# Optimization experiments

Hardware: AMD Instinct MI355X
Metric: run time of the kernel (lower is better)

## Reference

```python
import math
import jax, jax.numpy as jnp
import numpy as np
from jax import lax

N_HEADS = 8
FACTOR = 5


def _pos_emb(L, d):
    pos = jnp.arange(L, dtype=jnp.float32)[:, None]
    div = jnp.exp(jnp.arange(0, d, 2, dtype=jnp.float32) * (-math.log(10000.0) / d))
    pe = jnp.zeros((L, d), jnp.float32)
    pe = pe.at[:, 0::2].set(jnp.sin(pos * div))
    pe = pe.at[:, 1::2].set(jnp.cos(pos * div))
    return pe


def _circ_conv1d(x, w, b=None):
    # x: (B, L, Cin); w: torch conv1d weight (Cout, Cin, 3); circular padding=1
    xp = jnp.concatenate([x[:, -1:], x, x[:, :1]], axis=1)
    y = lax.conv_general_dilated(xp, jnp.transpose(w, (2, 1, 0)), (1,), 'VALID',
                                 dimension_numbers=('NWC', 'WIO', 'NWC'))
    return y + b if b is not None else y


def _ln(x, g, b, eps=1e-5):
    mu = x.mean(-1, keepdims=True)
    var = ((x - mu) ** 2).mean(-1, keepdims=True)
    return (x - mu) * lax.rsqrt(var + eps) * g + b


def _prob_attn(q, k, v, key):
    # q,k,v: (b, h, L, d); self-attention so l_q == l_k == L
    b, h, L, d = q.shape
    u = min(L, int(FACTOR * math.log(L + 1)))  # sample_k == n_top
    idx = jnp.asarray(jax.random.randint(key, (L, u), 0, L))  # shared across b,h as in torch

    # sampled QK scores: scan over the u samples to avoid a (b,h,L,u,d) gather blow-up
    def step(_, idx_s):
        kg = k[:, :, idx_s]  # (b,h,L,d): key idx_s[l] for query l
        return None, jnp.einsum('bhld,bhld->bhl', q, kg)
    _, qk = lax.scan(step, None, idx.T)  # (u, b, h, L)
    qk = jnp.moveaxis(qk, 0, -1)  # (b, h, L, u)

    m = qk.max(axis=-1) - qk.mean(axis=-1)  # sparsity measure, (b,h,L)
    _, top = lax.top_k(m, u)  # (b,h,u) top-u query indices

    q_red = jnp.take_along_axis(q, top[..., None], axis=2)  # (b,h,u,d)
    scores = jnp.einsum('bhud,bhkd->bhuk', q_red, k) * (1.0 / math.sqrt(d))
    attn = jax.nn.softmax(scores, axis=-1)
    ctx_top = jnp.einsum('bhuk,bhkd->bhud', attn, v)

    # non-selected queries get mean(V); scatter sparse-attention rows back in
    ctx = jnp.broadcast_to(v.mean(axis=2, keepdims=True), (b, h, L, d))
    bi = jnp.arange(b)[:, None, None]
    hi = jnp.arange(h)[None, :, None]
    return ctx.at[bi, hi, top].set(ctx_top)


def _attn_layer(x, wq, bq, wk, bk, wv, bv, wo, bo, key):
    b, L, dm = x.shape
    dh = dm // N_HEADS
    def split(w_, b_):
        return (x @ w_.T + b_).reshape(b, L, N_HEADS, dh).transpose(0, 2, 1, 3)
    ctx = _prob_attn(split(wq, bq), split(wk, bk), split(wv, bv), key)
    ctx = ctx.transpose(0, 2, 1, 3).reshape(b, L, dm)
    return ctx @ wo.T + bo


def _conv_layer(x, w, b, g, beta):
    # circular conv -> BatchNorm (batch stats, train-mode math) -> ELU -> maxpool k3 s2 p1
    y = _circ_conv1d(x, w, b)
    mu = y.mean(axis=(0, 1))
    var = y.var(axis=(0, 1))
    y = (y - mu) * lax.rsqrt(var + 1e-5) * g + beta
    y = jax.nn.elu(y)
    yp = jnp.pad(y, ((0, 0), (1, 1), (0, 0)), constant_values=-np.inf)
    return lax.reduce_window(yp, -np.inf, lax.max, (1, 3, 1), (1, 2, 1), 'VALID')


def _forward(x, skip_w, skip_b, token_conv_w, wq, bq, wk, bk, wv, bv, wo, bo,
             w1, b1, w2, b2, ln1_g, ln1_b, ln2_g, ln2_b,
             dc_w, dc_b, bn_g, bn_b, final_ln_g, final_ln_b, proj_w, proj_b):
    skip = x[:, -1] @ skip_w.T + skip_b  # (B, pred_len)
    h = _circ_conv1d(x, token_conv_w)  # token embedding (no bias)
    h = h + _pos_emb(h.shape[1], h.shape[2])
    E = wq.shape[0]
    base = jax.random.key(42)
    for i in range(E):
        new_h = _attn_layer(h, wq[i], bq[i], wk[i], bk[i], wv[i], bv[i], wo[i], bo[i],
                            jax.random.fold_in(base, i))
        h = h + new_h
        y = _ln(h, ln1_g[i], ln1_b[i])
        y = jax.nn.gelu(y @ w1[i].T + b1[i], approximate=False)  # conv1 is 1x1
        y = y @ w2[i].T + b2[i]  # conv2 is 1x1
        h = _ln(h + y, ln2_g[i], ln2_b[i])
        if i < E - 1:
            h = _conv_layer(h, dc_w[i], dc_b[i], bn_g[i], bn_b[i])  # halves L
    h = _ln(h, final_ln_g, final_ln_b)
    return h[:, -1] @ proj_w.T + proj_b + skip


def setup_inputs() -> dict:
    B, L, C_IN, D, DFF, E, P = 32, 2048, 7, 512, 2048, 3, 96
    key = jax.random.key(0)
    ks = iter(jax.random.split(key, 20))
    w = lambda shape: jax.random.normal(next(ks), shape, jnp.float32) * 0.02
    z = lambda shape: jnp.zeros(shape, jnp.float32)
    o = lambda shape: jnp.ones(shape, jnp.float32)
    return {
        'x': jax.random.normal(next(ks), (B, L, C_IN), jnp.float32),
        'skip_w': w((P, C_IN)), 'skip_b': z((P,)),
        'token_conv_w': w((D, C_IN, 3)),
        'wq': w((E, D, D)), 'bq': z((E, D)),
        'wk': w((E, D, D)), 'bk': z((E, D)),
        'wv': w((E, D, D)), 'bv': z((E, D)),
        'wo': w((E, D, D)), 'bo': z((E, D)),
        'w1': w((E, DFF, D)), 'b1': z((E, DFF)),
        'w2': w((E, D, DFF)), 'b2': z((E, D)),
        'ln1_g': o((E, D)), 'ln1_b': z((E, D)),
        'ln2_g': o((E, D)), 'ln2_b': z((E, D)),
        'dc_w': w((E - 1, D, D, 3)), 'dc_b': z((E - 1, D)),
        'bn_g': o((E - 1, D)), 'bn_b': z((E - 1, D)),
        'final_ln_g': o((D,)), 'final_ln_b': z((D,)),
        'proj_w': w((P, D)), 'proj_b': z((P,)),
    }


def reference(x, skip_w, skip_b, token_conv_w, wq, bq, wk, bk, wv, bv, wo, bo,
              w1, b1, w2, b2, ln1_g, ln1_b, ln2_g, ln2_b,
              dc_w, dc_b, bn_g, bn_b, final_ln_g, final_ln_b, proj_w, proj_b):
    return _forward(x, skip_w, skip_b, token_conv_w, wq, bq, wk, bk, wv, bv, wo, bo,
                    w1, b1, w2, b2, ln1_g, ln1_b, ln2_g, ln2_b,
                    dc_w, dc_b, bn_g, bn_b, final_ln_g, final_ln_b, proj_w, proj_b)
```

## Files before the change

### kernel.cpp

```cpp
#include <hip/hip_runtime.h>
#include <cmath>

#define DM 512
#define DH 64

typedef __attribute__((ext_vector_type(8))) short short8;
typedef __attribute__((ext_vector_type(4))) float float4v;

__device__ inline float b2f(unsigned short u){
  union{unsigned int i; float f;} z; z.i = ((unsigned)u)<<16; return z.f;
}
__device__ inline unsigned short f2b(float f){
  unsigned int x = __float_as_uint(f);
  return (unsigned short)((x + 0x7fffu + ((x>>16)&1u)) >> 16);
}

#define GLL(gp, lp) __builtin_amdgcn_global_load_lds((const __attribute__((address_space(1))) void*)(gp), \
    (__attribute__((address_space(3))) void*)(lp), 16, 0, 0)

__host__ __device__ inline void tf2x32(unsigned k0, unsigned k1, unsigned& x0, unsigned& x1){
  const unsigned ks0=k0, ks1=k1, ks2=k0^k1^0x1BD11BDAu;
  x0 += ks0; x1 += ks1;
#define TF_ROT(r) { x0 += x1; x1 = (x1<<(r))|(x1>>(32-(r))); x1 ^= x0; }
  TF_ROT(13) TF_ROT(15) TF_ROT(26) TF_ROT(6)
  x0 += ks1; x1 += ks2 + 1u;
  TF_ROT(17) TF_ROT(29) TF_ROT(16) TF_ROT(24)
  x0 += ks2; x1 += ks0 + 2u;
  TF_ROT(13) TF_ROT(15) TF_ROT(26) TF_ROT(6)
  x0 += ks0; x1 += ks1 + 3u;
  TF_ROT(17) TF_ROT(29) TF_ROT(16) TF_ROT(24)
  x0 += ks1; x1 += ks2 + 4u;
  TF_ROT(13) TF_ROT(15) TF_ROT(26) TF_ROT(6)
  x0 += ks2; x1 += ks0 + 5u;
#undef TF_ROT
}

__global__ __launch_bounds__(256) void idx_kernel(int* __restrict__ idx, unsigned k2a, unsigned k2b,
                                                  int S2, int Lmask){
  int j = blockIdx.x*256 + threadIdx.x;
  if (j >= S2) return;
  unsigned x0 = (unsigned)j, x1 = (unsigned)(S2 + j);
  tf2x32(k2a, k2b, x0, x1);
  idx[j]      = (int)(x0 & (unsigned)Lmask);
  idx[S2 + j] = (int)(x1 & (unsigned)Lmask);
}

__global__ __launch_bounds__(256) void pe_kernel(float* __restrict__ pe, int L){
  int i = blockIdx.x*256 + threadIdx.x;
  int d = i % DM, l = i / DM;
  const float scale = -0.017988946f;
  float freq = expf((float)(d & ~1) * scale);
  float ang  = (float)l * freq;
  pe[i] = (d & 1) ? cosf(ang) : sinf(ang);
}

__global__ __launch_bounds__(256) void embed_kernel(const float* __restrict__ x, const float* __restrict__ tcw,
                                                    const float* __restrict__ pe, float* __restrict__ h, int L){
  size_t i = (size_t)blockIdx.x*256 + threadIdx.x;
  int d = (int)(i % DM);
  size_t r = i / DM;
  int l = (int)(r % L);
  int b = (int)(r / L);
  const float* xb = x + (size_t)b*L*7;
  float acc = 0.f;
#pragma unroll
  for (int kk=0; kk<3; kk++){
    int ls = l + kk - 1;
    ls = (ls < 0) ? ls + L : (ls >= L ? ls - L : ls);
    const float* xe = xb + (size_t)ls*7;
    const float* wp = tcw + (size_t)d*21 + kk;
#pragma unroll
    for (int c=0;c<7;c++) acc += xe[c]*wp[3*c];
  }
  h[i] = acc + pe[(size_t)l*DM + d];
}

__global__ __launch_bounds__(256) void f2b_vec(const float* __restrict__ src, unsigned short* __restrict__ dst, int n4){
  int i = blockIdx.x*256 + threadIdx.x;
  if (i >= n4) return;
  float4 v = ((const float4*)src)[i];
  ushort4 o; o.x = f2b(v.x); o.y = f2b(v.y); o.z = f2b(v.z); o.w = f2b(v.w);
  ((ushort4*)dst)[i] = o;
}

__global__ __launch_bounds__(256) void packconv(const float* __restrict__ dcw, unsigned short* __restrict__ wtapK){
  int i = blockIdx.x*256 + threadIdx.x;
  if (i >= 3*DM*DM) return;
  int n = i / (3*DM); int rem = i % (3*DM); int tap = rem / DM; int c = rem % DM;
  wtapK[(size_t)n*(3*DM) + tap*DM + c] = f2b(dcw[((size_t)n*DM + c)*3 + tap]);
}

__global__ __launch_bounds__(256) void catb_kernel(const float* __restrict__ a, const float* __restrict__ b,
    const float* __restrict__ c, float* __restrict__ o){
  int i = blockIdx.x*256 + threadIdx.x;
  if (i >= 1536) return;
  o[i] = (i < 512) ? a[i] : (i < 1024 ? b[i-512] : c[i-1024]);
}

template<int TN, int A32>
__global__ __launch_bounds__(256) void bgemm2(const void* __restrict__ Ain,
    const unsigned short* __restrict__ Wb, const float* __restrict__ bias, void* __restrict__ C,
    int N, int K, int L, int convmode, int act, int outbf, int qkv, size_t bufstride, int swz){
  constexpr int NJ = TN/32;
  constexpr int BR = TN/32;
  __shared__ unsigned short As[128*64];
  __shared__ unsigned short Bs[TN*64];
  int tid = threadIdx.x;
  int w = tid >> 6, ln = tid & 63;

  int bx = blockIdx.x, by = blockIdx.y;
  if (swz){
    int XT = gridDim.x, YT = gridDim.y;
    int lid = by*XT + bx;
    int xcd = lid & 7, s = lid >> 3;
    int ych = YT >> 3;
    int CHv = ych < 16 ? ych : 16;
    int yloc = s % CHv;
    int t2 = s / CHv;
    int xx = t2 % XT;
    int chunk = t2 / XT;
    by = xcd*ych + chunk*CHv + yloc;
    bx = xx;
  }
  int row0 = by*128, col0 = bx*TN;
  int KA = convmode ? 512 : K;

  long aBase[4], dPrev[4], dNext[4]; int aCol[4];
#pragma unroll
  for (int g=0; g<4; g++){
    int ch = g*256 + tid;
    int r = ch >> 3, c = ch & 7;
    int gc = c ^ (r & 7);
    int gr = row0 + r;
    aCol[g] = gc*8;
    aBase[g] = (long)gr * KA;
    if (convmode){
      int l = gr % L;
      dPrev[g] = (l==0)   ? (long)(L-1)*KA : -(long)KA;
      dNext[g] = (l==L-1) ? -(long)(L-1)*KA : (long)KA;
    } else { dPrev[g]=0; dNext[g]=0; }
  }
  long bBase[BR];
#pragma unroll
  for (int g=0; g<BR; g++){
    int ch = g*256 + tid;
    int r = ch >> 3, c = ch & 7;
    int gc = c ^ (r & 7);
    bBase[g] = (long)(col0 + r)*K + gc*8;
  }
  int raBase[4], rbBase[NJ];
#pragma unroll
  for (int i=0;i<4;i++)  raBase[i] = ((w&1)*64 + i*16 + (ln&15))*8;
#pragma unroll
  for (int j=0;j<NJ;j++) rbBase[j] = ((w>>1)*(TN/2) + j*16 + (ln&15))*8;

  float4v acc[4][NJ] = {};
  int nIter = K/64;
  const unsigned short* A16 = (const unsigned short*)Ain;
  const float* Af = (const float*)Ain;

  for (int it=0; it<nIter; it++){
    int k0 = it*64;
    int kk = convmode ? (k0 & 511) : k0;
    int seg = convmode ? (k0 >> 9) : 1;
    if (A32){
#pragma unroll
      for (int g=0; g<4; g++){
        long d = convmode ? ((seg==0) ? dPrev[g] : (seg==2 ? dNext[g] : 0)) : 0;
        const float* src = Af + aBase[g] + d + kk + aCol[g];
        float4 v0 = *(const float4*)src;
        float4 v1 = *(const float4*)(src+4);
        short8 pk;
        pk[0]=(short)f2b(v0.x); pk[1]=(short)f2b(v0.y); pk[2]=(short)f2b(v0.z); pk[3]=(short)f2b(v0.w);
        pk[4]=(short)f2b(v1.x); pk[5]=(short)f2b(v1.y); pk[6]=(short)f2b(v1.z); pk[7]=(short)f2b(v1.w);
        *(short8*)((char*)As + g*4096 + tid*16) = pk;
      }
    } else {
#pragma unroll
      for (int g=0; g<4; g++){
        long d = convmode ? ((seg==0) ? dPrev[g] : (seg==2 ? dNext[g] : 0)) : 0;
        GLL(A16 + aBase[g] + d + kk + aCol[g], (char*)As + g*4096 + w*1024);
      }
    }
#pragma unroll
    for (int g=0; g<BR; g++)
      GLL(Wb + bBase[g] + k0, (char*)Bs + g*4096 + w*1024);
    __syncthreads();
    const char* ab = (const char*)As;
    const char* bb = (const char*)Bs;
#pragma unroll
    for (int s=0;s<2;s++){
      int xs = (s*4 + (ln>>4)) ^ (ln&7);
      short8 af[4], bf[NJ];
#pragma unroll
      for (int i=0;i<4;i++)  af[i] = *(const short8*)(ab + (raBase[i] + xs)*16);
#pragma unroll
      for (int j=0;j<NJ;j++) bf[j] = *(const short8*)(bb + (rbBase[j] + xs)*16);
#pragma unroll
      for (int i=0;i<4;i++)
#pragma unroll
        for (int j=0;j<NJ;j++)
          acc[i][j] = __builtin_amdgcn_mfma_f32_16x16x32_bf16(af[i], bf[j], acc[i][j], 0, 0, 0);
    }
    __syncthreads();
  }

  float* Cf = (float*)C;
  unsigned short* Cb = (unsigned short*)C;
  int colb0 = col0 + (w>>1)*(TN/2) + (ln & 15);
#pragma unroll
  for (int i=0;i<4;i++){
#pragma unroll
    for (int r=0;r<4;r++){
      int grow = row0 + (w&1)*64 + i*16 + (ln>>4)*4 + r;
#pragma unroll
      for (int j=0;j<NJ;j++){
        int colb = colb0 + j*16;
        float v = acc[i][j][r];
        if (bias) v += bias[colb];
        if (act)  v = 0.5f * v * (1.0f + erff(v * 0.70710678f));
        if (outbf){
          if (qkv){
            int bsel = colb >> 9;
            Cb[(size_t)bsel*bufstride + (size_t)grow*512 + (colb & 511)] = f2b(v);
          } else {
            Cb[(size_t)grow*N + colb] = f2b(v);
          }
        } else {
          Cf[(size_t)grow*N + colb] = v;
        }
      }
    }
  }
}

__global__ __launch_bounds__(256) void sample_m2(const unsigned short* __restrict__ q,
    const unsigned short* __restrict__ k, const int* __restrict__ idx, float* __restrict__ m, int L, int u){
  int w = (blockIdx.x*256 + threadIdx.x) >> 6;
  int lane = threadIdx.x & 63;
  int l = w % L; int b = w / L;
  const unsigned short* qrow = q + (size_t)w*DM + lane*8;
  uint4 qq = *(const uint4*)qrow;
  float qv[8];
  qv[0]=b2f((unsigned short)(qq.x&0xffff)); qv[1]=b2f((unsigned short)(qq.x>>16));
  qv[2]=b2f((unsigned short)(qq.y&0xffff)); qv[3]=b2f((unsigned short)(qq.y>>16));
  qv[4]=b2f((unsigned short)(qq.z&0xffff)); qv[5]=b2f((unsigned short)(qq.z>>16));
  qv[6]=b2f((unsigned short)(qq.w&0xffff)); qv[7]=b2f((unsigned short)(qq.w>>16));
  const unsigned short* kb = k + (size_t)b*L*DM + lane*8;
  const int* ip = idx + (size_t)l*u;
  float mx = -1e30f, sum = 0.f;
  for (int s=0; s<u; s++){
    int kp = ip[s];
    uint4 kk = *(const uint4*)(kb + (size_t)kp*DM);
    float p;
    p  = qv[0]*b2f((unsigned short)(kk.x&0xffff)) + qv[1]*b2f((unsigned short)(kk.x>>16));
    p += qv[2]*b2f((unsigned short)(kk.y&0xffff)) + qv[3]*b2f((unsigned short)(kk.y>>16));
    p += qv[4]*b2f((unsigned short)(kk.z&0xffff)) + qv[5]*b2f((unsigned short)(kk.z>>16));
    p += qv[6]*b2f((unsigned short)(kk.w&0xffff)) + qv[7]*b2f((unsigned short)(kk.w>>16));
    p += __shfl_xor(p, 1); p += __shfl_xor(p, 2); p += __shfl_xor(p, 4);
    mx = fmaxf(mx, p); sum += p;
  }
  if ((lane & 7) == 0){
    int hh = lane >> 3;
    m[((size_t)b*8 + hh)*L + l] = mx - sum/(float)u;
  }
}

__global__ __launch_bounds__(256) void topk_kernel(const float* __restrict__ m, int* __restrict__ top, int L, int u){
  int bh = blockIdx.x;
  const float* mm = m + (size_t)bh*L;
  __shared__ float vals[2048];
  __shared__ float rv[256];
  __shared__ int   ri[256];
  for (int i=threadIdx.x; i<L; i+=256) vals[i] = mm[i];
  __syncthreads();
  for (int it=0; it<u; it++){
    float bv = -1e30f; int bi = 0x7fffffff;
    for (int i=threadIdx.x; i<L; i+=256){
      float v = vals[i];
      if (v > bv || (v == bv && i < bi)) { bv = v; bi = i; }
    }
    rv[threadIdx.x] = bv; ri[threadIdx.x] = bi;
    __syncthreads();
    for (int s=128; s; s>>=1){
      if (threadIdx.x < s){
        float v = rv[threadIdx.x+s]; int i2 = ri[threadIdx.x+s];
        if (v > rv[threadIdx.x] || (v == rv[threadIdx.x] && i2 < ri[threadIdx.x])){
          rv[threadIdx.x] = v; ri[threadIdx.x] = i2;
        }
      }
      __syncthreads();
    }
    if (threadIdx.x == 0){ top[bh*u + it] = ri[0]; vals[ri[0]] = -1e31f; }
    __syncthreads();
  }
}

#define CMC 32
__global__ __launch_bounds__(256) void colmean1(const float* __restrict__ src, float* __restrict__ part, int L){
  int b = blockIdx.x, ch = blockIdx.y;
  int rpb = L / CMC;
  int t = threadIdx.x;
  const float* p = src + ((size_t)b*L + (size_t)ch*rpb)*DM;
  float s0 = 0.f, s1 = 0.f;
  for (int r=0; r<rpb; r++){ s0 += p[(size_t)r*DM + t]; s1 += p[(size_t)r*DM + t + 256]; }
  float* o = part + ((size_t)b*CMC + ch)*DM;
  o[t] = s0; o[t+256] = s1;
}
__global__ __launch_bounds__(256) void colmean2(const float* __restrict__ part, float* __restrict__ dst, int L){
  int i = blockIdx.x*256 + threadIdx.x;
  int d = i % DM, b = i / DM;
  float s = 0.f;
  for (int c=0; c<CMC; c++) s += part[((size_t)b*CMC + c)*DM + d];
  dst[i] = s / (float)L;
}

__global__ __launch_bounds__(256) void tiny_gemm(const float* __restrict__ A, const float* __restrict__ W,
    const float* __restrict__ bias, float* __restrict__ C, int N, int K){
  int row = blockIdx.x;
  const float* ar = A + (size_t)row*K;
  __shared__ float as[DM];
  for (int k=threadIdx.x; k<K; k+=256) as[k] = ar[k];
  __syncthreads();
  for (int n = threadIdx.x; n < N; n += 256){
    float acc = bias ? bias[n] : 0.f;
    const float* wr = W + (size_t)n*K;
    for (int k=0; k<K; k++) acc += as[k]*wr[k];
    C[(size_t)row*N + n] = acc;
  }
}

__global__ __launch_bounds__(256) void qred_kernel(const unsigned short* __restrict__ q, const int* __restrict__ top,
    float* __restrict__ qred, int L, int u, int n){
  int i = blockIdx.x*256 + threadIdx.x;
  if (i >= n) return;
  int d = i & 63; int rest = i >> 6; int j = rest % u; int bh = rest / u;
  int hh = bh & 7; int b = bh >> 3;
  int pos = top[bh*u + j];
  qred[i] = b2f(q[((size_t)b*L + pos)*DM + hh*DH + d]);
}

__global__ __launch_bounds__(256) void qk_scores(const float* __restrict__ qred,
    const unsigned short* __restrict__ kbuf, float* __restrict__ S, int L, int u){
  int bh = blockIdx.y; int b = bh >> 3, h = bh & 7;
  int key = blockIdx.x*256 + threadIdx.x;
  __shared__ float Qs[38*64];
  int t = threadIdx.x;
  for (int i = t; i < u*64; i += 256) Qs[i] = qred[(size_t)bh*u*64 + i];
  __syncthreads();
  const unsigned short* krow = kbuf + ((size_t)(b*L + key))*DM + h*DH;
  float kr[64];
#pragma unroll
  for (int c=0;c<8;c++){
    uint4 kk = *(const uint4*)(krow + c*8);
    kr[c*8+0]=b2f((unsigned short)(kk.x&0xffff)); kr[c*8+1]=b2f((unsigned short)(kk.x>>16));
    kr[c*8+2]=b2f((unsigned short)(kk.y&0xffff)); kr[c*8+3]=b2f((unsigned short)(kk.y>>16));
    kr[c*8+4]=b2f((unsigned short)(kk.z&0xffff)); kr[c*8+5]=b2f((unsigned short)(kk.z>>16));
    kr[c*8+6]=b2f((unsigned short)(kk.w&0xffff)); kr[c*8+7]=b2f((unsigned short)(kk.w>>16));
  }
  float* srow = S + (size_t)bh*u*L + key;
  for (int m = 0; m < u; m++){
    const float4* q4 = (const float4*)(Qs + m*64);
    float acc = 0.f;
#pragma unroll
    for (int c=0;c<16;c++){
      float4 qv = q4[c];
      acc += qv.x*kr[c*4] + qv.y*kr[c*4+1] + qv.z*kr[c*4+2] + qv.w*kr[c*4+3];
    }
    srow[(size_t)m*L] = acc * 0.125f;
  }
}

__global__ __launch_bounds__(256) void softmax_rows(float* __restrict__ S, int L){
  size_t row = blockIdx.x;
  float* r = S + row*(size_t)L;
  int t = threadIdx.x;
  __shared__ float red[8];
  float mx = -1e30f;
  for (int i=t;i<L;i+=256) mx = fmaxf(mx, r[i]);
#pragma unroll
  for (int off=32; off; off>>=1) mx = fmaxf(mx, __shfl_xor(mx, off));
  if ((t&63)==0) red[t>>6] = mx;
  __syncthreads();
  mx = fmaxf(fmaxf(red[0],red[1]), fmaxf(red[2],red[3]));
  float sum = 0.f;
  for (int i=t;i<L;i+=256){ float e = expf(r[i]-mx); r[i] = e; sum += e; }
#pragma unroll
  for (int off=32; off; off>>=1) sum += __shfl_xor(sum, off);
  if ((t&63)==0) red[4+(t>>6)] = sum;
  __syncthreads();
  float inv = 1.f/(red[4]+red[5]+red[6]+red[7]);
  for (int i=t;i<L;i+=256) r[i] *= inv;
}

#define PVKT 256
__global__ __launch_bounds__(256) void pv_kernel(const float* __restrict__ P,
    const unsigned short* __restrict__ vbuf, float* __restrict__ ctxt, int L, int u){
  int bh = blockIdx.y; int b = bh >> 3, h = bh & 7;
  int k0 = blockIdx.x*PVKT;
  int t = threadIdx.x;
  __shared__ unsigned short Vs[PVKT*64];
  for (int e = t*8; e < PVKT*64; e += 2048){
    int k = e>>6, d = e&63;
    *(uint4*)(Vs + e) = *(const uint4*)(vbuf + ((size_t)(b*L + k0 + k))*DM + h*DH + d);
  }
  __syncthreads();
  int n = t & 63, mg = t >> 6;
  for (int m = mg; m < u; m += 4){
    const float* prow = P + ((size_t)bh*u + m)*L + k0;
    float acc = 0.f;
    for (int k=0;k<PVKT;k+=4){
      float4 p4 = *(const float4*)(prow + k);
      acc += p4.x*b2f(Vs[(k+0)*64+n]);
      acc += p4.y*b2f(Vs[(k+1)*64+n]);
      acc += p4.z*b2f(Vs[(k+2)*64+n]);
      acc += p4.w*b2f(Vs[(k+3)*64+n]);
    }
    atomicAdd(&ctxt[((size_t)bh*u + m)*64 + n], acc);
  }
}

__global__ __launch_bounds__(256) void scatter_delta(const float* __restrict__ ctxt, const float* __restrict__ vmean,
    const float* __restrict__ wo, const int* __restrict__ top, float* __restrict__ h, int L, int u){
  int bid = blockIdx.x;
  int j = bid % u; int bh = bid / u; int hh = bh & 7; int b = bh >> 3;
  int pos = top[bh*u + j];
  __shared__ float delta[DH];
  int t = threadIdx.x;
  if (t < DH) delta[t] = ctxt[(size_t)(bh*u + j)*DH + t] - vmean[b*DM + hh*DH + t];
  __syncthreads();
  float* hrow = h + ((size_t)b*L + pos)*DM;
  const float* wbase = wo + hh*DH;
  for (int n = t; n < DM; n += 256){
    float acc = 0.f;
    const float* wr = wbase + (size_t)n*DM;
#pragma unroll
    for (int dd=0; dd<DH; dd++) acc += delta[dd] * wr[dd];
    atomicAdd(&hrow[n], acc);
  }
}

__global__ __launch_bounds__(256) void ln_kernel(const float* __restrict__ X, const void* __restrict__ Yadd,
    int yb, const float* __restrict__ g, const float* __restrict__ bta, void* __restrict__ Out, int ob,
    const float* __restrict__ cwv, int Lrow, int row0g){
  size_t row = blockIdx.x;
  const float* xr = X + row*DM;
  int t = threadIdx.x;
  float v0 = xr[t], v1 = xr[t+256];
  if (cwv){
    int b = (int)((row0g + (int)row) / Lrow);
    v0 += cwv[b*DM + t]; v1 += cwv[b*DM + t+256];
  }
  if (Yadd){
    if (yb){ const unsigned short* yr = (const unsigned short*)Yadd + row*DM; v0 += b2f(yr[t]); v1 += b2f(yr[t+256]); }
    else   { const float* yr = (const float*)Yadd + row*DM; v0 += yr[t]; v1 += yr[t+256]; }
  }
  float s = v0+v1, q = v0*v0+v1*v1;
#pragma unroll
  for (int off=32; off; off>>=1){ s += __shfl_xor(s,off); q += __shfl_xor(q,off); }
  __shared__ float ss[4], qq[4];
  int w = t >> 6;
  if ((t & 63) == 0){ ss[w] = s; qq[w] = q; }
  __syncthreads();
  s = ss[0]+ss[1]+ss[2]+ss[3]; q = qq[0]+qq[1]+qq[2]+qq[3];
  float mu  = s * (1.0f/DM);
  float var = q * (1.0f/DM) - mu*mu;
  float r = rsqrtf(var + 1e-5f);
  float o0 = (v0 - mu)*r*g[t]     + bta[t];
  float o1 = (v1 - mu)*r*g[t+256] + bta[t+256];
  if (ob){
    unsigned short* Ob = (unsigned short*)Out;
    Ob[row*DM + t] = f2b(o0); Ob[row*DM + t+256] = f2b(o1);
  } else {
    float* Of = (float*)Out;
    Of[row*DM + t] = o0; Of[row*DM + t+256] = o1;
  }
}

__global__ __launch_bounds__(256) void bnstat1(const unsigned short* __restrict__ C, float* __restrict__ partS,
                                               float* __restrict__ partQ, int rpb){
  int chb = blockIdx.x;
  int mb  = blockIdx.y;
  int g = threadIdx.x >> 6, c = threadIdx.x & 63;
  int ch = chb*64 + c;
  float s = 0.f, q = 0.f;
  int r0 = mb * rpb;
  for (int r = r0 + g; r < r0 + rpb; r += 4){
    float v = b2f(C[(size_t)r*DM + ch]); s += v; q += v*v;
  }
  __shared__ float ls[4][64], lq[4][64];
  ls[g][c] = s; lq[g][c] = q;
  __syncthreads();
  if (g == 0){
    s = ls[0][c]+ls[1][c]+ls[2][c]+ls[3][c];
    q = lq[0][c]+lq[1][c]+lq[2][c]+lq[3][c];
    partS[(size_t)mb*DM + ch] = s;
    partQ[(size_t)mb*DM + ch] = q;
  }
}
__global__ __launch_bounds__(256) void bnstat2(const float* __restrict__ partS, const float* __restrict__ partQ,
                                               float* __restrict__ stats, int NB, int M){
  int ch = blockIdx.x*256 + threadIdx.x;
  if (ch >= DM) return;
  float s = 0.f, q = 0.f;
  for (int mb=0; mb<NB; mb++){
    s += partS[(size_t)mb*DM + ch];
    q += partQ[(size_t)mb*DM + ch];
  }
  float mu = s / (float)M;
  stats[ch] = mu;
  stats[DM + ch] = q / (float)M - mu*mu;
}

__global__ __launch_bounds__(256) void bnpool(const unsigned short* __restrict__ C, const float* __restrict__ stats,
    const float* __restrict__ g, const float* __restrict__ bta, float* __restrict__ Out,
    int L, int Lo){
  size_t i = (size_t)blockIdx.x*256 + threadIdx.x;
  int ch = (int)(i % DM);
  size_t r = i / DM;
  int lo = (int)(r % Lo);
  int b  = (int)(r / Lo);
  float mu = stats[ch];
  float rstd = rsqrtf(stats[DM+ch] + 1e-5f);
  float gg = g[ch], bb = bta[ch];
  float best = -1e30f;
#pragma unroll
  for (int t=-1; t<=1; t++){
    int li = 2*lo + t;
    if (li >= 0 && li < L){
      float v = (b2f(C[((size_t)b*L + li)*DM + ch]) - mu)*rstd*gg + bb;
      v = v > 0.f ? v : expm1f(v);
      best = fmaxf(best, v);
    }
  }
  Out[((size_t)b*Lo + lo)*DM + ch] = best;
}

__global__ __launch_bounds__(128) void final_kernel(const float* __restrict__ h, const float* __restrict__ x,
    const float* __restrict__ fg, const float* __restrict__ fb, const float* __restrict__ pw,
    const float* __restrict__ pb, const float* __restrict__ sw, const float* __restrict__ sb,
    float* __restrict__ out, int Lf, int L0){
  int b = blockIdx.x;
  const float* row = h + ((size_t)b*Lf + (Lf-1))*DM;
  __shared__ float xn[DM];
  __shared__ float rs[2], rq[2];
  int t = threadIdx.x;
  float v[4]; float s = 0.f, q = 0.f;
#pragma unroll
  for (int i=0;i<4;i++){ v[i] = row[t + i*128]; s += v[i]; q += v[i]*v[i]; }
#pragma unroll
  for (int off=32; off; off>>=1){ s += __shfl_xor(s,off); q += __shfl_xor(q,off); }
  if ((t & 63) == 0){ rs[t>>6] = s; rq[t>>6] = q; }
  __syncthreads();
  s = rs[0]+rs[1]; q = rq[0]+rq[1];
  float mu = s*(1.0f/DM), var = q*(1.0f/DM) - mu*mu;
  float r = rsqrtf(var + 1e-5f);
#pragma unroll
  for (int i=0;i<4;i++){ int d = t + i*128; xn[d] = (v[i]-mu)*r*fg[d] + fb[d]; }
  __syncthreads();
  if (t < 96){
    float acc = pb[t] + sb[t];
    const float* xr = x + ((size_t)b*L0 + (L0-1))*7;
#pragma unroll
    for (int c=0;c<7;c++) acc += xr[c]*sw[t*7+c];
    for (int d=0; d<DM; d++) acc += xn[d]*pw[(size_t)t*DM + d];
    out[b*96 + t] = acc;
  }
}

extern "C" void kernel_launch(void* const* d_in, const int* in_sizes, int n_in,
                              void* d_out, int out_size, void* d_ws, size_t ws_size,
                              hipStream_t stream){
  const float* x    = (const float*)d_in[0];
  const float* skw  = (const float*)d_in[1];
  const float* skb  = (const float*)d_in[2];
  const float* tcw  = (const float*)d_in[3];
  const float* wq   = (const float*)d_in[4];
  const float* bq   = (const float*)d_in[5];
  const float* wk   = (const float*)d_in[6];
  const float* bk   = (const float*)d_in[7];
  const float* wv   = (const float*)d_in[8];
  const float* bv   = (const float*)d_in[9];
  const float* wo   = (const float*)d_in[10];
  const float* bo   = (const float*)d_in[11];
  const float* w1   = (const float*)d_in[12];
  const float* b1   = (const float*)d_in[13];
  const float* w2   = (const float*)d_in[14];
  const float* b2   = (const float*)d_in[15];
  const float* ln1g = (const float*)d_in[16];
  const float* ln1b = (const float*)d_in[17];
  const float* ln2g = (const float*)d_in[18];
  const float* ln2b = (const float*)d_in[19];
  const float* dcw  = (const float*)d_in[20];
  const float* dcb  = (const float*)d_in[21];
  const float* bng  = (const float*)d_in[22];
  const float* bnb  = (const float*)d_in[23];
  const float* flg  = (const float*)d_in[24];
  const float* flb  = (const float*)d_in[25];
  const float* pw   = (const float*)d_in[26];
  const float* pb   = (const float*)d_in[27];

  const int B = 32, L0 = 2048, DFF = 2048;
  const int RG = 16384;
  const int RF = 8192;
  char* ws = (char*)d_ws;
  const size_t SZH  = (size_t)B*L0*DM*sizeof(float);
  const size_t SLOT = (size_t)RG*DM*sizeof(unsigned short);

  const size_t WBSZ = (size_t)(3*DM*DM + 2*DFF*DM + 3*DM*DM)*2;
  size_t small_bytes = (size_t)L0*40*4
                     + (size_t)RG*8*4
                     + (size_t)B*8*40*4
                     + (size_t)32*8*40*64*4
                     + (size_t)32*8*40*64*4
                     + 3*(size_t)B*DM*4
                     + 2*(size_t)128*DM*4
                     + (size_t)2*DM*4
                     + (size_t)1536*4
                     + (size_t)B*CMC*DM*4
                     + (size_t)L0*DM*4;
  if (ws_size < SZH + 4*SLOT + WBSZ + small_bytes) return;

  float*          h   = (float*)(ws);
  unsigned short* P0  = (unsigned short*)(ws + SZH);
  unsigned short* P1  = (unsigned short*)(ws + SZH + SLOT);
  unsigned short* P2  = (unsigned short*)(ws + SZH + 2*SLOT);
  unsigned short* P3  = (unsigned short*)(ws + SZH + 3*SLOT);
  unsigned short* wb  = (unsigned short*)(ws + SZH + 4*SLOT);
  unsigned short* wqb = wb;
  unsigned short* w1b = wqb + (size_t)3*DM*DM;
  unsigned short* w2b = w1b + (size_t)DFF*DM;
  unsigned short* wtapK= w2b + (size_t)DM*DFF;
  char* sm = ws + SZH + 4*SLOT + WBSZ;
  int*   idx_buf  = (int*)sm;
  float* m_buf    = (float*)(sm + (size_t)L0*40*4);
  int*   top_all  = (int*)((char*)m_buf + (size_t)RG*8*4);
  float* qred_loc = (float*)((char*)top_all + (size_t)B*8*40*4);
  float* ctxt_all = qred_loc + (size_t)32*8*40*64;
  float* hm       = ctxt_all + (size_t)32*8*40*64;
  float* vmean    = hm + (size_t)B*DM;
  float* cw       = vmean + (size_t)B*DM;
  float* partS    = cw + (size_t)B*DM;
  float* partQ    = partS + (size_t)128*DM;
  float* stats    = partQ + (size_t)128*DM;
  float* bqkv     = stats + (size_t)2*DM;
  float* partC    = bqkv + (size_t)1536;
  float* pe_buf   = partC + (size_t)B*CMC*DM;

  auto conv_b = [&](const float* src, unsigned short* dst, size_t n){
    f2b_vec<<<(int)((n/4 + 255)/256), 256, 0, stream>>>(src, dst, (int)(n/4));
  };

  pe_kernel<<<(int)(((size_t)L0*DM)/256), 256, 0, stream>>>(pe_buf, L0);
  embed_kernel<<<(int)(((size_t)B*L0*DM)/256), 256, 0, stream>>>(x, tcw, pe_buf, h, L0);

  int L = L0;
  const int SGtab[3] = {4, 8, 16};
  for (int layer = 0; layer < 3; layer++){
    int M = B * L;
    int u = (int)(5.0 * log((double)L + 1.0));
    int G = RG / L;
    int nG = M / RG;
    const float* wv_i = wv + (size_t)layer*DM*DM;  const float* bv_i = bv + (size_t)layer*DM;
    const float* wo_i = wo + (size_t)layer*DM*DM;  const float* bo_i = bo + (size_t)layer*DM;
    const float* b1_i = b1 + (size_t)layer*DFF;
    const float* b2_i = b2 + (size_t)layer*DM;

    conv_b(wq + (size_t)layer*DM*DM, wqb,                    (size_t)DM*DM);
    conv_b(wk + (size_t)layer*DM*DM, wqb + (size_t)DM*DM,    (size_t)DM*DM);
    conv_b(wv_i,                     wqb + (size_t)2*DM*DM,  (size_t)DM*DM);
    conv_b(w1 + (size_t)layer*DFF*DM, w1b, (size_t)DFF*DM);
    conv_b(w2 + (size_t)layer*DM*DFF, w2b, (size_t)DM*DFF);
    catb_kernel<<<6, 256, 0, stream>>>(bq + (size_t)layer*DM, bk + (size_t)layer*DM, bv_i, bqkv);
    if (layer < 2)
      packconv<<<(3*DM*DM + 255)/256, 256, 0, stream>>>(dcw + (size_t)layer*DM*DM*3, wtapK);

    unsigned ka = 0u, kb2 = (unsigned)layer;
    tf2x32(0u, 42u, ka, kb2);
    unsigned a0 = 0u, a1 = 2u;  tf2x32(ka, kb2, a0, a1);
    unsigned c0 = 1u, c1 = 3u;  tf2x32(ka, kb2, c0, c1);
    int S2 = L * u / 2;
    idx_kernel<<<(S2 + 255)/256, 256, 0, stream>>>(idx_buf, a1, c1, S2, L-1);

    hipMemsetAsync(ctxt_all, 0, (size_t)B*8*u*64*sizeof(float), stream);

    int sg = SGtab[layer];
    for (int g = 0; g < nG; g++){
      const float* hg = h + (size_t)g*RG*DM;
      bgemm2<128,1><<<dim3(12, RG/128), 256, 0, stream>>>(hg, wqb, bqkv, P1,
          1536, 512, L, 0, 0, 1, 1, (size_t)RG*DM, 1);
      sample_m2<<<RG/4, 256, 0, stream>>>(P1, P2, idx_buf, m_buf, L, u);
      int* top_g = top_all + (size_t)g*G*8*u;
      topk_kernel<<<G*8, 256, 0, stream>>>(m_buf, top_g, L, u);
      int nqr = G*8*u*DH;
      qred_kernel<<<(nqr + 255)/256, 256, 0, stream>>>(P1, top_g, qred_loc, L, u, nqr);

      float* Sbuf = (float*)P0;
      int nsub = G / sg;
      for (int s = 0; s < nsub; s++){
        const float* qr = qred_loc + (size_t)s*sg*8*u*64;
        const unsigned short* kb_ = P2 + (size_t)s*sg*L*DM;
        const unsigned short* vb_ = P3 + (size_t)s*sg*L*DM;
        float* ct = ctxt_all + (size_t)(g*G + s*sg)*8*u*64;
        qk_scores<<<dim3(L/256, sg*8), 256, 0, stream>>>(qr, kb_, Sbuf, L, u);
        softmax_rows<<<sg*8*u, 256, 0, stream>>>(Sbuf, L);
        pv_kernel<<<dim3(L/PVKT, sg*8), 256, 0, stream>>>(Sbuf, vb_, ct, L, u);
      }
    }

    colmean1<<<dim3(B, CMC), 256, 0, stream>>>(h, partC, L);
    colmean2<<<B*DM/256, 256, 0, stream>>>(partC, hm, L);
    tiny_gemm<<<B, 256, 0, stream>>>(hm, wv_i, bv_i, vmean, DM, DM);
    tiny_gemm<<<B, 256, 0, stream>>>(vmean, wo_i, bo_i, cw, DM, DM);

    scatter_delta<<<B*8*u, 256, 0, stream>>>(ctxt_all, vmean, wo_i, top_all, h, L, u);

    unsigned short* ybuf = P0;
    unsigned short* mid  = P1;
    unsigned short* y2b  = P0 + (size_t)RF*DM;
    const float* l1g = ln1g + (size_t)layer*DM; const float* l1b = ln1b + (size_t)layer*DM;
    const float* l2g = ln2g + (size_t)layer*DM; const float* l2b = ln2b + (size_t)layer*DM;
    for (int r0 = 0; r0 < M; r0 += RF){
      ln_kernel<<<RF, 256, 0, stream>>>(h + (size_t)r0*DM, nullptr, 0, l1g, l1b, ybuf, 1, cw, L, r0);
      bgemm2<128,0><<<dim3(16, RF/128), 256, 0, stream>>>(ybuf, w1b, b1_i, mid,
          2048, 512, L, 0, 1, 1, 0, 0, 1);
      bgemm2<64,0><<<dim3(8, RF/128), 256, 0, stream>>>(mid, w2b, b2_i, y2b,
          512, 2048, L, 0, 0, 1, 0, 0, 1);
      ln_kernel<<<RF, 256, 0, stream>>>(h + (size_t)r0*DM, y2b, 1, l2g, l2b, h + (size_t)r0*DM, 0, cw, L, r0);
    }

    if (layer < 2){
      const float* db = dcb + (size_t)layer*DM;
      unsigned short* convb = P0;
      bgemm2<64,1><<<dim3(8, M/128), 256, 0, stream>>>(h, wtapK, db, convb,
          512, 1536, L, 1, 0, 1, 0, 0, 1);
      bnstat1<<<dim3(8, 128), 256, 0, stream>>>(convb, partS, partQ, M/128);
      bnstat2<<<2, 256, 0, stream>>>(partS, partQ, stats, 128, M);
      int Lo = L/2;
      bnpool<<<(int)(((size_t)B*Lo*DM)/256), 256, 0, stream>>>(convb, stats,
          bng + (size_t)layer*DM, bnb + (size_t)layer*DM, h, L, Lo);
      L = Lo;
    }
  }

  final_kernel<<<B, 128, 0, stream>>>(h, x, flg, flb, pw, pb, skw, skb, (float*)d_out, L, L0);
}
```

Baseline: 5.686 ms.

## Fuse sparse-attention QK, softmax and PV into split-K flash kernel with merge

Replaces the separate qk_scores, softmax_rows and pv_kernel passes, which wrote full score rows to global memory, with one flash-style kernel. Each block handles one key split, keeps online softmax state in registers, and writes partial max, sum and accumulator values that a small merge kernel combines. This removes the global score buffer round-trips, the atomics and the memset. It also rewrites the embedding as one block per row reading a transposed weight, and swaps the erf GELU for a tanh approximation, which changes numerics slightly.

Result: faster. 5.426 ms (-4.6%).

```diff
diff --git a/kernel.cpp b/kernel.cpp
--- a/kernel.cpp
+++ b/kernel.cpp
@@ -54,25 +54,30 @@
   pe[i] = (d & 1) ? cosf(ang) : sinf(ang);
 }
 
-__global__ __launch_bounds__(256) void embed_kernel(const float* __restrict__ x, const float* __restrict__ tcw,
-                                                    const float* __restrict__ pe, float* __restrict__ h, int L){
-  size_t i = (size_t)blockIdx.x*256 + threadIdx.x;
-  int d = (int)(i % DM);
-  size_t r = i / DM;
-  int l = (int)(r % L);
-  int b = (int)(r / L);
-  const float* xb = x + (size_t)b*L*7;
-  float acc = 0.f;
-#pragma unroll
-  for (int kk=0; kk<3; kk++){
-    int ls = l + kk - 1;
-    ls = (ls < 0) ? ls + L : (ls >= L ? ls - L : ls);
-    const float* xe = xb + (size_t)ls*7;
-    const float* wp = tcw + (size_t)d*21 + kk;
-#pragma unroll
-    for (int c=0;c<7;c++) acc += xe[c]*wp[3*c];
-  }
-  h[i] = acc + pe[(size_t)l*DM + d];
+__global__ __launch_bounds__(256) void packtcw(const float* __restrict__ tcw, float* __restrict__ tcwT){
+  int i = blockIdx.x*256 + threadIdx.x;
+  if (i >= 21*DM) return;
+  int j = i / DM, d = i % DM;
+  tcwT[(size_t)j*DM + d] = tcw[(size_t)d*21 + (j%7)*3 + (j/7)];
+}
+
+__global__ __launch_bounds__(256) void embed2(const float* __restrict__ x, const float* __restrict__ tcwT,
+                                              const float* __restrict__ pe, float* __restrict__ h, int L){
+  int row = blockIdx.x; int l = row % L, b = row / L;
+  __shared__ float xs[21];
+  int t = threadIdx.x;
+  if (t < 21){
+    int c = t % 7, kk = t / 7;
+    int ls = l + kk - 1; ls = (ls < 0) ? ls + L : (ls >= L ? ls - L : ls);
+    xs[t] = x[((size_t)b*L + ls)*7 + c];
+  }
+  __syncthreads();
+  for (int d = t; d < DM; d += 256){
+    float acc = 0.f;
+#pragma unroll
+    for (int j=0;j<21;j++) acc += xs[j]*tcwT[j*DM + d];
+    h[(size_t)row*DM + d] = acc + pe[(size_t)l*DM + d];
+  }
 }
 
 __global__ __launch_bounds__(256) void f2b_vec(const float* __restrict__ src, unsigned short* __restrict__ dst, int n4){
@@ -218,7 +223,11 @@
         int colb = colb0 + j*16;
         float v = acc[i][j][r];
         if (bias) v += bias[colb];
-        if (act)  v = 0.5f * v * (1.0f + erff(v * 0.70710678f));
+        if (act){
+          float z = 0.7978845608f * v * (1.f + 0.044715f*v*v);
+          float e = __expf(2.f*z);
+          v = v * (1.f - 1.f/(e + 1.f));
+        }
         if (outbf){
           if (qkv){
             int bsel = colb >> 9;
@@ -340,84 +349,96 @@
   qred[i] = b2f(q[((size_t)b*L + pos)*DM + hh*DH + d]);
 }
 
-__global__ __launch_bounds__(256) void qk_scores(const float* __restrict__ qred,
-    const unsigned short* __restrict__ kbuf, float* __restrict__ S, int L, int u){
-  int bh = blockIdx.y; int b = bh >> 3, h = bh & 7;
-  int key = blockIdx.x*256 + threadIdx.x;
+#define FKT 128
+__global__ __launch_bounds__(256) void flash_attn(const float* __restrict__ qred,
+    const unsigned short* __restrict__ kbuf, const unsigned short* __restrict__ vbuf,
+    float* __restrict__ partM, float* __restrict__ partL, float* __restrict__ partA,
+    int L, int u, int KS){
+  int ks = blockIdx.x, bh = blockIdx.y; int b = bh >> 3, h = bh & 7;
+  int t = threadIdx.x;
   __shared__ float Qs[38*64];
-  int t = threadIdx.x;
-  for (int i = t; i < u*64; i += 256) Qs[i] = qred[(size_t)bh*u*64 + i];
-  __syncthreads();
-  const unsigned short* krow = kbuf + ((size_t)(b*L + key))*DM + h*DH;
-  float kr[64];
-#pragma unroll
-  for (int c=0;c<8;c++){
-    uint4 kk = *(const uint4*)(krow + c*8);
-    kr[c*8+0]=b2f((unsigned short)(kk.x&0xffff)); kr[c*8+1]=b2f((unsigned short)(kk.x>>16));
-    kr[c*8+2]=b2f((unsigned short)(kk.y&0xffff)); kr[c*8+3]=b2f((unsigned short)(kk.y>>16));
-    kr[c*8+4]=b2f((unsigned short)(kk.z&0xffff)); kr[c*8+5]=b2f((unsigned short)(kk.z>>16));
-    kr[c*8+6]=b2f((unsigned short)(kk.w&0xffff)); kr[c*8+7]=b2f((unsigned short)(kk.w>>16));
-  }
-  float* srow = S + (size_t)bh*u*L + key;
-  for (int m = 0; m < u; m++){
-    const float4* q4 = (const float4*)(Qs + m*64);
-    float acc = 0.f;
-#pragma unroll
-    for (int c=0;c<16;c++){
-      float4 qv = q4[c];
-      acc += qv.x*kr[c*4] + qv.y*kr[c*4+1] + qv.z*kr[c*4+2] + qv.w*kr[c*4+3];
-    }
-    srow[(size_t)m*L] = acc * 0.125f;
-  }
-}
-
-__global__ __launch_bounds__(256) void softmax_rows(float* __restrict__ S, int L){
-  size_t row = blockIdx.x;
-  float* r = S + row*(size_t)L;
-  int t = threadIdx.x;
-  __shared__ float red[8];
-  float mx = -1e30f;
-  for (int i=t;i<L;i+=256) mx = fmaxf(mx, r[i]);
-#pragma unroll
-  for (int off=32; off; off>>=1) mx = fmaxf(mx, __shfl_xor(mx, off));
-  if ((t&63)==0) red[t>>6] = mx;
-  __syncthreads();
-  mx = fmaxf(fmaxf(red[0],red[1]), fmaxf(red[2],red[3]));
-  float sum = 0.f;
-  for (int i=t;i<L;i+=256){ float e = expf(r[i]-mx); r[i] = e; sum += e; }
-#pragma unroll
-  for (int off=32; off; off>>=1) sum += __shfl_xor(sum, off);
-  if ((t&63)==0) red[4+(t>>6)] = sum;
-  __syncthreads();
-  float inv = 1.f/(red[4]+red[5]+red[6]+red[7]);
-  for (int i=t;i<L;i+=256) r[i] *= inv;
-}
-
-#define PVKT 256
-__global__ __launch_bounds__(256) void pv_kernel(const float* __restrict__ P,
-    const unsigned short* __restrict__ vbuf, float* __restrict__ ctxt, int L, int u){
-  int bh = blockIdx.y; int b = bh >> 3, h = bh & 7;
-  int k0 = blockIdx.x*PVKT;
-  int t = threadIdx.x;
-  __shared__ unsigned short Vs[PVKT*64];
-  for (int e = t*8; e < PVKT*64; e += 2048){
-    int k = e>>6, d = e&63;
-    *(uint4*)(Vs + e) = *(const uint4*)(vbuf + ((size_t)(b*L + k0 + k))*DM + h*DH + d);
-  }
-  __syncthreads();
-  int n = t & 63, mg = t >> 6;
-  for (int m = mg; m < u; m += 4){
-    const float* prow = P + ((size_t)bh*u + m)*L + k0;
-    float acc = 0.f;
-    for (int k=0;k<PVKT;k+=4){
-      float4 p4 = *(const float4*)(prow + k);
-      acc += p4.x*b2f(Vs[(k+0)*64+n]);
-      acc += p4.y*b2f(Vs[(k+1)*64+n]);
-      acc += p4.z*b2f(Vs[(k+2)*64+n]);
-      acc += p4.w*b2f(Vs[(k+3)*64+n]);
-    }
-    atomicAdd(&ctxt[((size_t)bh*u + m)*64 + n], acc);
-  }
+  __shared__ unsigned short Ks[FKT*64];
+  __shared__ unsigned short Vs[FKT*64];
+  __shared__ float Ss[38*FKT];
+  for (int i=t;i<u*64;i+=256) Qs[i] = qred[(size_t)bh*u*64 + i];
+  int lane = t & 63, w = t >> 6;
+  float rm[10], rl[10], racc[10];
+#pragma unroll
+  for (int j=0;j<10;j++){ rm[j]=-1e30f; rl[j]=0.f; racc[j]=0.f; }
+  int nk = L / KS;
+  int kbase = ks*nk;
+  int key = t & 127, rh = t >> 7;
+  for (int kt = 0; kt < nk; kt += FKT){
+    __syncthreads();
+    for (int e = t; e < FKT*8; e += 256){
+      int k = e >> 3, c = e & 7;
+      size_t gidx = ((size_t)(b*L + kbase + kt + k))*DM + h*DH + c*8;
+      *(uint4*)((char*)Ks + (size_t)(k*8 + (c ^ (k&7)))*16) = *(const uint4*)(kbuf + gidx);
+      *(uint4*)((char*)Vs + (size_t)e*16) = *(const uint4*)(vbuf + gidx);
+    }
+    __syncthreads();
+    for (int r = rh; r < u; r += 2){
+      const float4* q4 = (const float4*)(Qs + r*64);
+      float acc = 0.f;
+#pragma unroll
+      for (int c=0;c<8;c++){
+        short8 kk = *(const short8*)((char*)Ks + (size_t)(key*8 + (c ^ (key&7)))*16);
+        float4 qa = q4[c*2], qb = q4[c*2+1];
+        acc += qa.x*b2f((unsigned short)kk[0]) + qa.y*b2f((unsigned short)kk[1])
+             + qa.z*b2f((unsigned short)kk[2]) + qa.w*b2f((unsigned short)kk[3]);
+        acc += qb.x*b2f((unsigned short)kk[4]) + qb.y*b2f((unsigned short)kk[5])
+             + qb.z*b2f((unsigned short)kk[6]) + qb.w*b2f((unsigned short)kk[7]);
+      }
+      Ss[r*FKT + key] = acc * 0.125f;
+    }
+    __syncthreads();
+    int j = 0;
+    for (int r = w; r < u; r += 4, j++){
+      float s0 = Ss[r*FKT + lane], s1 = Ss[r*FKT + 64 + lane];
+      float mx = fmaxf(s0, s1);
+#pragma unroll
+      for (int off=32; off; off>>=1) mx = fmaxf(mx, __shfl_xor(mx, off));
+      float newm = fmaxf(rm[j], mx);
+      float scale = expf(rm[j] - newm);
+      float p0 = expf(s0 - newm), p1 = expf(s1 - newm);
+      float ps = p0 + p1;
+#pragma unroll
+      for (int off=32; off; off>>=1) ps += __shfl_xor(ps, off);
+      rl[j] = rl[j]*scale + ps;
+      rm[j] = newm;
+      Ss[r*FKT + lane] = p0; Ss[r*FKT + 64 + lane] = p1;
+      float a = racc[j]*scale;
+      for (int k=0;k<FKT;k+=4){
+        float pa = Ss[r*FKT+k], pb = Ss[r*FKT+k+1], pc = Ss[r*FKT+k+2], pd = Ss[r*FKT+k+3];
+        a += pa*b2f(Vs[(k+0)*64+lane]) + pb*b2f(Vs[(k+1)*64+lane])
+           + pc*b2f(Vs[(k+2)*64+lane]) + pd*b2f(Vs[(k+3)*64+lane]);
+      }
+      racc[j] = a;
+    }
+  }
+  int j = 0;
+  for (int r = w; r < u; r += 4, j++){
+    size_t base = ((size_t)bh*KS + ks)*u + r;
+    if (lane == 0){ partM[base] = rm[j]; partL[base] = rl[j]; }
+    partA[base*64 + lane] = racc[j];
+  }
+}
+
+__global__ __launch_bounds__(256) void flash_merge(const float* __restrict__ partM, const float* __restrict__ partL,
+    const float* __restrict__ partA, float* __restrict__ ctxt, int u, int KS, int n){
+  int i = blockIdx.x*256 + threadIdx.x;
+  if (i >= n) return;
+  int nn = i & 63; int rest = i >> 6; int r = rest % u; int bhl = rest / u;
+  size_t base0 = ((size_t)bhl*KS)*u + r;
+  float gm = -1e30f;
+  for (int s=0;s<KS;s++) gm = fmaxf(gm, partM[base0 + (size_t)s*u]);
+  float lt = 0.f, at = 0.f;
+  for (int s=0;s<KS;s++){
+    float e = expf(partM[base0 + (size_t)s*u] - gm);
+    lt += partL[base0 + (size_t)s*u]*e;
+    at += partA[(base0 + (size_t)s*u)*64 + nn]*e;
+  }
+  ctxt[i] = at / lt;
 }
 
 __global__ __launch_bounds__(256) void scatter_delta(const float* __restrict__ ctxt, const float* __restrict__ vmean,
@@ -618,7 +639,8 @@
                      + (size_t)2*DM*4
                      + (size_t)1536*4
                      + (size_t)B*CMC*DM*4
-                     + (size_t)L0*DM*4;
+                     + (size_t)L0*DM*4
+                     + (size_t)21*DM*4;
   if (ws_size < SZH + 4*SLOT + WBSZ + small_bytes) return;
 
   float*          h   = (float*)(ws);
@@ -646,21 +668,27 @@
   float* bqkv     = stats + (size_t)2*DM;
   float* partC    = bqkv + (size_t)1536;
   float* pe_buf   = partC + (size_t)B*CMC*DM;
+  float* tcwT     = pe_buf + (size_t)L0*DM;
+
+  float* fpM = (float*)P0;
+  float* fpL = fpM + (size_t)256*40;
+  float* fpA = fpL + (size_t)256*40;
 
   auto conv_b = [&](const float* src, unsigned short* dst, size_t n){
     f2b_vec<<<(int)((n/4 + 255)/256), 256, 0, stream>>>(src, dst, (int)(n/4));
   };
 
   pe_kernel<<<(int)(((size_t)L0*DM)/256), 256, 0, stream>>>(pe_buf, L0);
-  embed_kernel<<<(int)(((size_t)B*L0*DM)/256), 256, 0, stream>>>(x, tcw, pe_buf, h, L0);
+  packtcw<<<(21*DM + 255)/256, 256, 0, stream>>>(tcw, tcwT);
+  embed2<<<B*L0, 256, 0, stream>>>(x, tcwT, pe_buf, h, L0);
 
   int L = L0;
-  const int SGtab[3] = {4, 8, 16};
   for (int layer = 0; layer < 3; layer++){
     int M = B * L;
     int u = (int)(5.0 * log((double)L + 1.0));
     int G = RG / L;
     int nG = M / RG;
+    int KS = L / 512;
     const float* wv_i = wv + (size_t)layer*DM*DM;  const float* bv_i = bv + (size_t)layer*DM;
     const float* wo_i = wo + (size_t)layer*DM*DM;  const float* bo_i = bo + (size_t)layer*DM;
     const float* b1_i = b1 + (size_t)layer*DFF;
@@ -682,9 +710,6 @@
     int S2 = L * u / 2;
     idx_kernel<<<(S2 + 255)/256, 256, 0, stream>>>(idx_buf, a1, c1, S2, L-1);
 
-    hipMemsetAsync(ctxt_all, 0, (size_t)B*8*u*64*sizeof(float), stream);
-
-    int sg = SGtab[layer];
     for (int g = 0; g < nG; g++){
       const float* hg = h + (size_t)g*RG*DM;
       bgemm2<128,1><<<dim3(12, RG/128), 256, 0, stream>>>(hg, wqb, bqkv, P1,
@@ -695,17 +720,10 @@
       int nqr = G*8*u*DH;
       qred_kernel<<<(nqr + 255)/256, 256, 0, stream>>>(P1, top_g, qred_loc, L, u, nqr);
 
-      float* Sbuf = (float*)P0;
-      int nsub = G / sg;
-      for (int s = 0; s < nsub; s++){
-        const float* qr = qred_loc + (size_t)s*sg*8*u*64;
-        const unsigned short* kb_ = P2 + (size_t)s*sg*L*DM;
-        const unsigned short* vb_ = P3 + (size_t)s*sg*L*DM;
-        float* ct = ctxt_all + (size_t)(g*G + s*sg)*8*u*64;
-        qk_scores<<<dim3(L/256, sg*8), 256, 0, stream>>>(qr, kb_, Sbuf, L, u);
-        softmax_rows<<<sg*8*u, 256, 0, stream>>>(Sbuf, L);
-        pv_kernel<<<dim3(L/PVKT, sg*8), 256, 0, stream>>>(Sbuf, vb_, ct, L, u);
-      }
+      flash_attn<<<dim3(KS, G*8), 256, 0, stream>>>(qred_loc, P2, P3, fpM, fpL, fpA, L, u, KS);
+      int nmg = G*8*u*64;
+      flash_merge<<<(nmg + 255)/256, 256, 0, stream>>>(fpM, fpL, fpA,
+          ctxt_all + (size_t)g*G*8*u*64, u, KS, nmg);
     }
 
     colmean1<<<dim3(B, CMC), 256, 0, stream>>>(h, partC, L);
```
